# Performance work log

Measured on AMD Instinct MI355X. Metric: run time of the kernel, lower is better.

## Reference

```python
import jax, jax.numpy as jnp
import numpy as np

H = 256        # h_dim
ATTN = 3       # attn_len (structurally fixed: 3 modality pairs / 3 unimodal streams)


def lstm_scan(x, Wih, Whh, b, h0, c0):
    """Standard LSTM (PyTorch gate order i,f,g,o) over time. x: (B,T,D) -> (B,T,H)."""
    def step(carry, xt):
        h, c = carry
        g = xt @ Wih + h @ Whh + b
        i, f, gg, o = jnp.split(g, 4, axis=-1)
        c = jax.nn.sigmoid(f) * c + jax.nn.sigmoid(i) * jnp.tanh(gg)
        h = jax.nn.sigmoid(o) * jnp.tanh(c)
        return (h, c), h
    _, hs = jax.lax.scan(step, (h0, c0), jnp.swapaxes(x, 0, 1))
    return jnp.swapaxes(hs, 0, 1)


def pad_shift(x, shift, padv=0.0):
    """Shift 3D tensor (B,T,D) forward in time by `shift` with constant padding."""
    pad = jnp.full((x.shape[0], shift, x.shape[2]), padv, x.dtype)
    return jnp.concatenate([pad, x[:, :-shift, :]], axis=1)


def setup_inputs() -> dict:
    key = jax.random.key(0)
    ks = jax.random.split(key, 24)
    B, T = 16, 1024
    F, A, Tx = 512, 256, 768
    s = jnp.float32(0.05)
    f32 = jnp.float32
    inp = {
        "x": jax.random.normal(ks[0], (B, T, 1), f32),
        "face_features": jax.random.normal(ks[1], (B, T, F), f32),
        "audio_features": jax.random.normal(ks[2], (B, T, A), f32),
        "text_features": jax.random.normal(ks[3], (B, T, Tx), f32),
        "target": jax.random.normal(ks[4], (B, T, 1), f32),
        "text_W": jax.random.normal(ks[5], (Tx, H), f32) * s,
        "text_b": jnp.zeros((H,), f32),
        "face_W": jax.random.normal(ks[6], (F, H), f32) * s,
        "face_b": jnp.zeros((H,), f32),
        "audio_W": jax.random.normal(ks[7], (A, H), f32) * s,
        "audio_b": jnp.zeros((H,), f32),
        "att_W": jax.random.normal(ks[8], (2 * H,), f32) * s,
        "att_b": jnp.zeros((), f32),
        "ut_W": jax.random.normal(ks[9], (H,), f32) * s,
        "ut_b": jnp.zeros((), f32),
        "uf_W": jax.random.normal(ks[10], (H,), f32) * s,
        "uf_b": jnp.zeros((), f32),
        "ua_W": jax.random.normal(ks[11], (H,), f32) * s,
        "ua_b": jnp.zeros((), f32),
        "enc_Wih": jax.random.normal(ks[12], (ATTN, ATTN, 4 * H), f32) * s,
        "enc_Whh": jax.random.normal(ks[13], (ATTN, H, 4 * H), f32) * s,
        "enc_b": jnp.zeros((ATTN, 4 * H), f32),
        "enc_outW": jax.random.normal(ks[14], (ATTN, H), f32) * s,
        "enc_outb": jnp.zeros((ATTN,), f32),
        "dec_Wih": jax.random.normal(ks[15], (1 + ATTN, 4 * H), f32) * s,
        "dec_Whh": jax.random.normal(ks[16], (H, 4 * H), f32) * s,
        "dec_b": jnp.zeros((4 * H,), f32),
        "dec_h0": jnp.zeros((H,), f32),
        "dec_c0": jnp.zeros((H,), f32),
        "out1_W": jax.random.normal(ks[17], (H, 4), f32) * s,
        "out1_b": jnp.zeros((4,), f32),
        "out2_W": jax.random.normal(ks[18], (4, 1), f32) * s,
        "out2_b": jnp.zeros((1,), f32),
    }
    return inp


def reference(x, face_features, audio_features, text_features, target,
              text_W, text_b, face_W, face_b, audio_W, audio_b,
              att_W, att_b, ut_W, ut_b, uf_W, uf_b, ua_W, ua_b,
              enc_Wih, enc_Whh, enc_b, enc_outW, enc_outb,
              dec_Wih, dec_Whh, dec_b, dec_h0, dec_c0,
              out1_W, out1_b, out2_W, out2_b):
    B, T = x.shape[0], x.shape[1]
    tr = text_features @ text_W + text_b    # (B,T,H)
    fr = face_features @ face_W + face_b
    ar = audio_features @ audio_W + audio_b

    def pair_att(a, b2):  # Linear(2H->1) on tanh(cat), softmax over TIME
        s = jnp.tanh(jnp.concatenate([a, b2], axis=-1)) @ att_W + att_b  # (B,T)
        return jax.nn.softmax(s, axis=-1)

    def uni(rep, W, bb):  # Linear(H->1) on tanh(rep), softmax over TIME
        return jax.nn.softmax(jnp.tanh(rep) @ W + bb, axis=-1)  # (B,T)

    att1 = pair_att(tr, fr); att2 = pair_att(fr, ar); att3 = pair_att(tr, ar)
    enc_input = jnp.concatenate([uni(tr, ut_W, ut_b), uni(fr, uf_W, uf_b),
                                 uni(ar, ua_W, ua_b)], axis=-1).reshape(B, T, ATTN)
    attn = jnp.concatenate([att1, att2, att3], axis=-1).reshape(B, T, ATTN)

    # cLSTM shared encoder: ATTN independent LSTMs over the full 3-dim input,
    # each followed by Linear(H->1); outputs concatenated -> (B,T,ATTN).
    z0 = jnp.zeros((B, H), enc_input.dtype)
    hs = jax.vmap(lambda Wih, Whh, bb: lstm_scan(enc_input, Wih, Whh, bb, z0, z0))(
        enc_Wih, enc_Whh, enc_b)                      # (ATTN,B,T,H)
    enc_out = jnp.einsum('kbth,kh->btk', hs, enc_outW) + enc_outb  # (B,T,ATTN)

    # convolve: local causal weighted sum over ATTN shifted copies
    shifted = jnp.stack([enc_out if i == 0 else pad_shift(enc_out, i)
                         for i in range(ATTN)], axis=-1)           # (B,T,ATTN,ATTN)
    context = jnp.sum(attn[:, :, None, :] * shifted, axis=-1)      # (B,T,ATTN)

    # decoder (teacher forcing path)
    dec_in = jnp.concatenate([pad_shift(target, 1, 0.0), context], axis=2)  # (B,T,1+ATTN)
    dh0 = jnp.tile(dec_h0[None], (B, 1))
    dc0 = jnp.tile(dec_c0[None], (B, 1))
    dec_out = lstm_scan(dec_in, dec_Wih, dec_Whh, dec_b, dh0, dc0)  # (B,T,H)
    predicted = jax.nn.relu(dec_out @ out1_W + out1_b) @ out2_W + out2_b  # (B,T,1)
    return predicted
```

## Files before the change

kernel.cpp:

```cpp
#include <hip/hip_runtime.h>
#include <hip/hip_bf16.h>

typedef float f32x4 __attribute__((ext_vector_type(4)));
typedef __bf16 bf16x8 __attribute__((ext_vector_type(8)));
typedef unsigned long long ull;

#define DEVI static __device__ __forceinline__

DEVI unsigned f2bfu(float f){
  unsigned u = __builtin_bit_cast(unsigned, f);
  return (u + 0x7fffu + ((u >> 16) & 1u)) >> 16;
}
DEVI float bf2f(unsigned s){
  return __builtin_bit_cast(float, s << 16);
}
DEVI float sigf(float x){ return 1.f/(1.f + __expf(-x)); }
DEVI float thf(float x){ return 2.f*sigf(2.f*x) - 1.f; }

DEVI ull allc(const ull* p){
  return __hip_atomic_load(p, __ATOMIC_RELAXED, __HIP_MEMORY_SCOPE_AGENT);
}
DEVI void alst(ull* p, ull v){
  __hip_atomic_store(p, v, __ATOMIC_RELAXED, __HIP_MEMORY_SCOPE_AGENT);
}

__global__ __launch_bounds__(256) void k_pack_lstm(
    const float* __restrict__ encWhh, const float* __restrict__ encWih,
    const float* __restrict__ decWhh, const float* __restrict__ decWih,
    const float* __restrict__ encB,   const float* __restrict__ decB,
    unsigned short* __restrict__ outp)
{
  const int total = 4*16*9*4*64*8;
  for (int e = blockIdx.x*blockDim.x + threadIdx.x; e < total; e += gridDim.x*blockDim.x){
    int j  = e & 7;
    int l  = (e >> 3) & 63;
    int g  = (e >> 9) & 3;
    int r  = e >> 11;
    int kt = r % 9;  r /= 9;
    int w  = r & 15;
    int lstm = r >> 4;
    int k = 32*kt + 8*(l >> 4) + j;
    int n = 256*g + 16*w + (l & 15);
    float v = 0.f;
    if (lstm < 3){
      if (k < 256)       v = encWhh[(lstm*256 + k)*1024 + n];
      else if (k < 259)  v = encWih[(lstm*3 + (k-256))*1024 + n];
      else if (k == 260) v = encB[lstm*1024 + n];
    } else {
      if (k < 256)       v = decWhh[k*1024 + n];
      else if (k < 260)  v = decWih[(k-256)*1024 + n];
      else if (k == 260) v = decB[n];
    }
    outp[e] = (unsigned short)f2bfu(v);
  }
}

__global__ __launch_bounds__(256) void k_pack_B(
    const float* __restrict__ W, int KT, unsigned short* __restrict__ outp)
{
  const int total = 2*KT*8*64*8;
  for (int e = blockIdx.x*blockDim.x + threadIdx.x; e < total; e += gridDim.x*blockDim.x){
    int j  = e & 7;
    int l  = (e >> 3) & 63;
    int nt = (e >> 9) & 7;
    int r  = e >> 12;
    int kt = r % KT;
    int tn = r / KT;
    int k = 32*kt + 8*(l >> 4) + j;
    int n = 128*tn + 16*nt + (l & 15);
    outp[e] = (unsigned short)f2bfu(W[k*256 + n]);
  }
}

__global__ __launch_bounds__(256) void k_proj(
    const float* __restrict__ A, const unsigned short* __restrict__ Bp,
    const float* __restrict__ bias, unsigned short* __restrict__ outT, int K)
{
  __shared__ unsigned char sA[8192];
  __shared__ unsigned char sB[8192];
  const int tid = threadIdx.x;
  const int l = tid & 63;
  const int wv = tid >> 6;
  const int wm = wv >> 1, wn = wv & 1;
  const int tm = blockIdx.x, tn = blockIdx.y;
  const int KT = K >> 5;

  f32x4 acc[4][4];
  #pragma unroll
  for (int a = 0; a < 4; ++a)
    #pragma unroll
    for (int cc = 0; cc < 4; ++cc)
      acc[a][cc] = f32x4{0.f,0.f,0.f,0.f};

  const int arow = tid >> 1;
  const float* Ap = A + (size_t)(tm*128 + arow)*K + (tid & 1)*16;
  const uint4* Bsrc = (const uint4*)Bp + (size_t)tn*KT*512 + tid*2;

  for (int kt = 0; kt < KT; ++kt){
    float4 f0 = *(const float4*)(Ap + kt*32);
    float4 f1 = *(const float4*)(Ap + kt*32 + 4);
    float4 f2 = *(const float4*)(Ap + kt*32 + 8);
    float4 f3 = *(const float4*)(Ap + kt*32 + 12);
    uint4 p0, p1;
    p0.x = f2bfu(f0.x) | (f2bfu(f0.y) << 16);
    p0.y = f2bfu(f0.z) | (f2bfu(f0.w) << 16);
    p0.z = f2bfu(f1.x) | (f2bfu(f1.y) << 16);
    p0.w = f2bfu(f1.z) | (f2bfu(f1.w) << 16);
    p1.x = f2bfu(f2.x) | (f2bfu(f2.y) << 16);
    p1.y = f2bfu(f2.z) | (f2bfu(f2.w) << 16);
    p1.z = f2bfu(f3.x) | (f2bfu(f3.y) << 16);
    p1.w = f2bfu(f3.z) | (f2bfu(f3.w) << 16);
    unsigned base = arow*64 + (tid & 1)*32;
    unsigned sw = (arow & 3) << 4;
    *(uint4*)(sA + ((base)      ^ sw)) = p0;
    *(uint4*)(sA + ((base + 16) ^ sw)) = p1;
    *((uint4*)sB + tid*2)     = Bsrc[kt*512];
    *((uint4*)sB + tid*2 + 1) = Bsrc[kt*512 + 1];
    __syncthreads();

    bf16x8 af[4], bf[4];
    #pragma unroll
    for (int a = 0; a < 4; ++a){
      unsigned row = 64*wm + 16*a + (l & 15);
      unsigned off = (row*64 + 16*(l >> 4)) ^ ((row & 3) << 4);
      af[a] = __builtin_bit_cast(bf16x8, *(const uint4*)(sA + off));
    }
    #pragma unroll
    for (int cc = 0; cc < 4; ++cc){
      unsigned off = ((4*wn + cc)*64 + l)*16;
      bf[cc] = __builtin_bit_cast(bf16x8, *(const uint4*)(sB + off));
    }
    #pragma unroll
    for (int a = 0; a < 4; ++a)
      #pragma unroll
      for (int cc = 0; cc < 4; ++cc)
        acc[a][cc] = __builtin_amdgcn_mfma_f32_16x16x32_bf16(af[a], bf[cc], acc[a][cc], 0, 0, 0);
    __syncthreads();
  }
  #pragma unroll
  for (int cc = 0; cc < 4; ++cc){
    int colg = tn*128 + 64*wn + 16*cc + (l & 15);
    float bs = bias[colg];
    #pragma unroll
    for (int a = 0; a < 4; ++a){
      int rowg = tm*128 + 64*wm + 16*a + 4*(l >> 4);
      #pragma unroll
      for (int r = 0; r < 4; ++r){
        outT[(size_t)(rowg + r)*256 + colg] = (unsigned short)f2bfu(thf(acc[a][cc][r] + bs));
      }
    }
  }
}

__global__ __launch_bounds__(256) void k_attdot(
    const unsigned short* __restrict__ tT, const unsigned short* __restrict__ tF,
    const unsigned short* __restrict__ tA,
    const float* __restrict__ attW, const float* __restrict__ utW,
    const float* __restrict__ ufW, const float* __restrict__ uaW,
    float* __restrict__ s6)
{
  const int l = threadIdx.x & 63;
  const int wid = (blockIdx.x*blockDim.x + threadIdx.x) >> 6;
  const int nw = (gridDim.x*blockDim.x) >> 6;
  float alo[4], ahi[4], wt[4], wf[4], wa[4];
  #pragma unroll
  for (int q = 0; q < 4; ++q){
    alo[q] = attW[4*l + q];
    ahi[q] = attW[256 + 4*l + q];
    wt[q]  = utW[4*l + q];
    wf[q]  = ufW[4*l + q];
    wa[q]  = uaW[4*l + q];
  }
  for (int r = wid; r < 16384; r += nw){
    uint2 vT = *(const uint2*)(tT + (size_t)r*256 + 4*l);
    uint2 vF = *(const uint2*)(tF + (size_t)r*256 + 4*l);
    uint2 vA = *(const uint2*)(tA + (size_t)r*256 + 4*l);
    float xt[4] = { bf2f(vT.x & 0xffff), bf2f(vT.x >> 16), bf2f(vT.y & 0xffff), bf2f(vT.y >> 16) };
    float xf[4] = { bf2f(vF.x & 0xffff), bf2f(vF.x >> 16), bf2f(vF.y & 0xffff), bf2f(vF.y >> 16) };
    float xa[4] = { bf2f(vA.x & 0xffff), bf2f(vA.x >> 16), bf2f(vA.y & 0xffff), bf2f(vA.y >> 16) };
    float ptlo = 0.f, ptu = 0.f, pflo = 0.f, pfhi = 0.f, pfu = 0.f, pahi = 0.f, pau = 0.f;
    #pragma unroll
    for (int q = 0; q < 4; ++q){
      ptlo += xt[q]*alo[q]; ptu += xt[q]*wt[q];
      pflo += xf[q]*alo[q]; pfhi += xf[q]*ahi[q]; pfu += xf[q]*wf[q];
      pahi += xa[q]*ahi[q]; pau += xa[q]*wa[q];
    }
    #pragma unroll
    for (int s = 1; s < 64; s <<= 1){
      ptlo += __shfl_xor(ptlo, s); ptu  += __shfl_xor(ptu, s);
      pflo += __shfl_xor(pflo, s); pfhi += __shfl_xor(pfhi, s);
      pfu  += __shfl_xor(pfu, s);  pahi += __shfl_xor(pahi, s);
      pau  += __shfl_xor(pau, s);
    }
    if (l == 0){
      int o = r;
      s6[o]             = ptlo + pfhi;
      s6[16384 + o]     = pflo + pahi;
      s6[2*16384 + o]   = ptlo + pahi;
      s6[3*16384 + o]   = ptu;
      s6[4*16384 + o]   = pfu;
      s6[5*16384 + o]   = pau;
    }
  }
}

__global__ __launch_bounds__(256) void k_zerofeed(unsigned short* __restrict__ encfeed)
{
  int i = blockIdx.x*blockDim.x + threadIdx.x;
  if (i < 16384) encfeed[i*4 + 3] = 0;
}

__global__ __launch_bounds__(256) void k_zerows(uint4* __restrict__ p, int n)
{
  for (int i = blockIdx.x*blockDim.x + threadIdx.x; i < n; i += gridDim.x*blockDim.x)
    p[i] = uint4{0u,0u,0u,0u};
}

__global__ __launch_bounds__(256) void k_smax(
    const float* __restrict__ s6, float* __restrict__ attn_tb,
    unsigned short* __restrict__ encfeed)
{
  __shared__ float red[4];
  const int f = blockIdx.x >> 4;
  const int b = blockIdx.x & 15;
  const int tid = threadIdx.x;
  const float* row = s6 + f*16384 + b*1024;
  float4 v = *(const float4*)(row + 4*tid);
  float mx = fmaxf(fmaxf(v.x, v.y), fmaxf(v.z, v.w));
  #pragma unroll
  for (int s = 1; s < 64; s <<= 1) mx = fmaxf(mx, __shfl_xor(mx, s));
  if ((tid & 63) == 0) red[tid >> 6] = mx;
  __syncthreads();
  mx = fmaxf(fmaxf(red[0], red[1]), fmaxf(red[2], red[3]));
  float e0 = __expf(v.x - mx), e1 = __expf(v.y - mx), e2 = __expf(v.z - mx), e3 = __expf(v.w - mx);
  float sm = e0 + e1 + e2 + e3;
  __syncthreads();
  #pragma unroll
  for (int s = 1; s < 64; s <<= 1) sm += __shfl_xor(sm, s);
  if ((tid & 63) == 0) red[tid >> 6] = sm;
  __syncthreads();
  sm = red[0] + red[1] + red[2] + red[3];
  float inv = 1.f/sm;
  float e[4] = {e0, e1, e2, e3};
  int ff = (f < 3) ? f : f - 3;
  #pragma unroll
  for (int q = 0; q < 4; ++q){
    int idx = ff*1024 + 4*tid + q;
    int tt = idx/3, kk = idx - 3*tt;
    if (f < 3) attn_tb[(tt*16 + b)*3 + kk] = e[q]*inv;
    else       encfeed[(tt*16 + b)*4 + kk] = (unsigned short)f2bfu(e[q]*inv);
  }
}

__global__ __launch_bounds__(512, 2) void k_lstm(
    const unsigned short* __restrict__ packW,
    const unsigned short* __restrict__ encfeed,
    const float* __restrict__ target,
    const float* __restrict__ attn_tb,
    const float* __restrict__ encOutW,
    const float* __restrict__ encOutB,
    const float* __restrict__ dec_h0,
    const float* __restrict__ dec_c0,
    unsigned short* __restrict__ dec_h,
    ull* __restrict__ exch,
    ull* __restrict__ partials)
{
  __shared__ unsigned char hl[2][16*768];
  __shared__ float ring[3][16][3];
  __shared__ float eo_part[2][48];
  const int tid = threadIdx.x;
  const int l = tid & 63;
  const int w = tid >> 6;
  const int pair = blockIdx.x >> 1;
  const int half = blockIdx.x & 1;
  const int wglob = half*8 + w;
  const bool isdec = (pair == 3);

  const int b = l & 15;
  const int j0 = 16*wglob + 4*(l >> 4);
  const unsigned swb = (unsigned)(b & 7) << 4;

  float c[4];
  #pragma unroll
  for (int r = 0; r < 4; ++r) c[r] = isdec ? dec_c0[j0 + r] : 0.f;

  float wow[4] = {0.f, 0.f, 0.f, 0.f};
  if (!isdec){
    #pragma unroll
    for (int r = 0; r < 4; ++r) wow[r] = encOutW[pair*256 + j0 + r];
  }
  float eb[3] = {0.f, 0.f, 0.f};
  if (isdec && tid < 16){
    #pragma unroll
    for (int k = 0; k < 3; ++k) eb[k] = encOutB[k];
  }

  {
    int ib = tid >> 5;
    int ic = (tid & 31) * 8;
    #pragma unroll
    for (int q = 0; q < 2; ++q){
      int c0 = ic + 4*q;
      uint2 hz;
      if (isdec){
        hz.x = f2bfu(dec_h0[c0])   | (f2bfu(dec_h0[c0+1]) << 16);
        hz.y = f2bfu(dec_h0[c0+2]) | (f2bfu(dec_h0[c0+3]) << 16);
      } else { hz.x = 0u; hz.y = 0u; }
      *(uint2*)(hl[0] + ((ib*768 + 2*c0) ^ ((unsigned)(ib & 7) << 4))) = hz;
    }
  }
  if (tid < 224){
    int bufi = tid / 112;
    int r = tid % 112;
    int bb = r / 7, q = r % 7;
    uint2 z;
    z.x = (q == 0) ? 0x00003f80u : 0u;
    z.y = 0u;
    *(uint2*)(hl[bufi] + ((bb*768 + 520 + 8*q) ^ ((unsigned)(bb & 7) << 4))) = z;
  }
  if (!isdec && tid < 16){
    uint2 gx0 = *(const uint2*)(encfeed + tid*4);
    *(uint2*)(hl[0] + ((tid*768 + 512) ^ ((unsigned)(tid & 7) << 4))) = gx0;
  }

  const uint4* wb = (const uint4*)packW + ((size_t)(pair*16 + wglob)*36)*64 + l;
  uint4 wreg[36];
  #pragma unroll
  for (int i = 0; i < 36; ++i) wreg[i] = wb[i*64];
  #pragma unroll
  for (int i = 0; i < 36; ++i){
    unsigned t0 = wreg[i].x, t1 = wreg[i].y, t2 = wreg[i].z, t3 = wreg[i].w;
    asm volatile("" : "+a"(t0), "+a"(t1), "+a"(t2), "+a"(t3));
    wreg[i].x = t0; wreg[i].y = t1; wreg[i].z = t2; wreg[i].w = t3;
  }

  if (isdec){
    if (tid < 96){
      int bb = tid & 15, kk = (tid >> 4) % 3, h2 = tid / 48;
      const ull* p8 = partials + (((size_t)0*3 + kk)*2 + h2)*128 + bb;
      ull v[8];
      #pragma unroll
      for (int wv = 0; wv < 8; ++wv) v[wv] = allc(p8 + wv*16);
      bool ok = false;
      while (!ok){
        ok = true;
        #pragma unroll
        for (int wv = 0; wv < 8; ++wv)
          if ((unsigned)(v[wv] >> 32) != 1u){ v[wv] = allc(p8 + wv*16); ok = false; }
      }
      float s = 0.f;
      #pragma unroll
      for (int wv = 0; wv < 8; ++wv) s += __builtin_bit_cast(float, (unsigned)v[wv]);
      eo_part[h2][kk*16 + bb] = s;
    }
    __syncthreads();
    if (tid < 16){
      int bb = tid;
      float a0 = attn_tb[bb*3 + 0];
      unsigned ok3[3];
      #pragma unroll
      for (int k = 0; k < 3; ++k){
        float eo = eb[k] + eo_part[0][k*16 + bb] + eo_part[1][k*16 + bb];
        ring[0][bb][k] = eo; ring[1][bb][k] = 0.f; ring[2][bb][k] = 0.f;
        ok3[k] = f2bfu(a0*eo);
      }
      uint2 pk; pk.x = (ok3[0] << 16); pk.y = ok3[1] | (ok3[2] << 16);
      *(uint2*)(hl[0] + ((bb*768 + 512) ^ ((unsigned)(bb & 7) << 4))) = pk;
    }
  }
  __syncthreads();

  for (int t = 0; t < 1024; ++t){
    const int p = t + 1;
    const unsigned char* cur = hl[t & 1];
    unsigned char* nxt = (unsigned char*)hl[p & 1];

    bf16x8 af[9];
    #pragma unroll
    for (int kt = 0; kt < 9; ++kt){
      unsigned off = (unsigned)(b*768 + kt*64 + 16*(l >> 4)) ^ swb;
      af[kt] = __builtin_bit_cast(bf16x8, *(const uint4*)(cur + off));
    }

    uint2 gx;
    const bool ldx = (!isdec) && (t < 1023) && (tid < 16);
    if (ldx) gx = *(const uint2*)(encfeed + (size_t)p*64 + tid*4);
    float at0 = 0.f, at1 = 0.f, at2 = 0.f, tg = 0.f;
    const bool bld = isdec && (t < 1023) && (tid < 16);
    if (bld){
      at0 = attn_tb[((size_t)p*16 + tid)*3 + 0];
      at1 = attn_tb[((size_t)p*16 + tid)*3 + 1];
      at2 = attn_tb[((size_t)p*16 + tid)*3 + 2];
      tg  = target[tid*1024 + t];
    }

    f32x4 acc[4];
    #pragma unroll
    for (int g = 0; g < 4; ++g) acc[g] = f32x4{0.f,0.f,0.f,0.f};
    #pragma unroll
    for (int kt = 0; kt < 9; ++kt){
      #pragma unroll
      for (int g = 0; g < 4; ++g)
        acc[g] = __builtin_amdgcn_mfma_f32_16x16x32_bf16(
            __builtin_bit_cast(bf16x8, wreg[kt*4 + g]), af[kt], acc[g], 0, 0, 0);
    }

    unsigned hp[4];
    #pragma unroll
    for (int r = 0; r < 4; ++r){
      float vi = sigf(acc[0][r]);
      float vf = sigf(acc[1][r]);
      float vg = thf (acc[2][r]);
      float vo = sigf(acc[3][r]);
      float cc = vf*c[r] + vi*vg;
      c[r] = cc;
      hp[r] = f2bfu(vo * thf(cc));
    }
    uint2 hpk; hpk.x = hp[0] | (hp[1] << 16); hpk.y = hp[2] | (hp[3] << 16);
    *(uint2*)(nxt + ((b*768 + 2*j0) ^ swb)) = hpk;

    if (isdec){
      *(uint2*)(dec_h + (size_t)(t*16 + b)*256 + j0) = hpk;
    } else {
      float s = bf2f(hp[0])*wow[0] + bf2f(hp[1])*wow[1]
              + bf2f(hp[2])*wow[2] + bf2f(hp[3])*wow[3];
      s += __shfl_xor(s, 16);
      s += __shfl_xor(s, 32);
      if (l < 16)
        alst(partials + (((size_t)t*3 + pair)*2 + half)*128 + w*16 + l,
             ((ull)(unsigned)p << 32) | (ull)__builtin_bit_cast(unsigned, s));
    }

    if (t < 1023){
      {
        size_t xs = ((((size_t)pair*2 + (p & 1))*2 + half)*16 + b)*64
                  + ((unsigned)(j0 & 127) >> 1);
        alst(exch + xs,     ((ull)(unsigned)p << 32) | (ull)hpk.x);
        alst(exch + xs + 1, ((ull)(unsigned)p << 32) | (ull)hpk.y);
      }
      const int pb2 = tid >> 5, pj = tid & 31;
      const ull* rb = exch + ((((size_t)pair*2 + (p & 1))*2 + (half^1))*16 + pb2)*64 + pj*2;
      ull v0 = allc(rb), v1 = allc(rb + 1);
      const bool pol = isdec && (tid < 96);
      const int kk = (tid >> 4) % 3, h2 = tid / 48, bb = tid & 15;
      const ull* p8 = partials + (((size_t)p*3 + kk)*2 + h2)*128 + bb;
      ull pv[8];
      if (pol){
        #pragma unroll
        for (int wv = 0; wv < 8; ++wv) pv[wv] = allc(p8 + wv*16);
      }
      while (((unsigned)(v0 >> 32) != (unsigned)p) || ((unsigned)(v1 >> 32) != (unsigned)p)){
        if ((unsigned)(v0 >> 32) != (unsigned)p) v0 = allc(rb);
        if ((unsigned)(v1 >> 32) != (unsigned)p) v1 = allc(rb + 1);
      }
      uint2 pk2; pk2.x = (unsigned)v0; pk2.y = (unsigned)v1;
      *(uint2*)(nxt + ((pb2*768 + 256*(half^1) + 8*pj) ^ ((unsigned)(pb2 & 7) << 4))) = pk2;
      if (pol){
        const unsigned want = (unsigned)(p + 1);
        bool ok = false;
        while (!ok){
          ok = true;
          #pragma unroll
          for (int wv = 0; wv < 8; ++wv)
            if ((unsigned)(pv[wv] >> 32) != want){ pv[wv] = allc(p8 + wv*16); ok = false; }
        }
        float s2 = 0.f;
        #pragma unroll
        for (int wv = 0; wv < 8; ++wv) s2 += __builtin_bit_cast(float, (unsigned)pv[wv]);
        eo_part[h2][kk*16 + bb] = s2;
      }
      if (ldx) *(uint2*)(nxt + ((tid*768 + 512) ^ ((unsigned)(tid & 7) << 4))) = gx;
      __syncthreads();
      if (isdec){
        if (tid < 16){
          int s0 = p % 3, s1 = (p + 2) % 3, s2i = (p + 1) % 3;
          unsigned ok3[3];
          #pragma unroll
          for (int k = 0; k < 3; ++k){
            float eo = eb[k] + eo_part[0][k*16 + tid] + eo_part[1][k*16 + tid];
            ring[s0][tid][k] = eo;
            ok3[k] = f2bfu(at0*eo + at1*ring[s1][tid][k] + at2*ring[s2i][tid][k]);
          }
          uint2 pk3; pk3.x = f2bfu(tg) | (ok3[0] << 16); pk3.y = ok3[1] | (ok3[2] << 16);
          *(uint2*)(nxt + ((tid*768 + 512) ^ ((unsigned)(tid & 7) << 4))) = pk3;
        }
        __syncthreads();
      }
    }
  }
}

__global__ __launch_bounds__(256) void k_decout(
    const unsigned short* __restrict__ dec_h, const float* __restrict__ W1,
    const float* __restrict__ b1, const float* __restrict__ W2,
    const float* __restrict__ b2, float* __restrict__ out)
{
  const int l = threadIdx.x & 63;
  const int wid = (blockIdx.x*blockDim.x + threadIdx.x) >> 6;
  const int nw = (gridDim.x*blockDim.x) >> 6;
  const int o = l >> 4, jc = l & 15;
  for (int e = wid; e < 16384; e += nw){
    int t = e >> 4, b = e & 15;
    const unsigned short* hr = dec_h + (size_t)(t*16 + b)*256 + jc*16;
    uint4 v0 = *(const uint4*)hr;
    uint4 v1 = *(const uint4*)(hr + 8);
    unsigned vv[8] = {v0.x, v0.y, v0.z, v0.w, v1.x, v1.y, v1.z, v1.w};
    float p = 0.f;
    #pragma unroll
    for (int q = 0; q < 8; ++q){
      int j = jc*16 + 2*q;
      p += bf2f(vv[q] & 0xffff) * W1[j*4 + o];
      p += bf2f(vv[q] >> 16)    * W1[(j + 1)*4 + o];
    }
    p += __shfl_xor(p, 1); p += __shfl_xor(p, 2);
    p += __shfl_xor(p, 4); p += __shfl_xor(p, 8);
    float v = 0.f;
    if (jc == 0) v = fmaxf(p + b1[o], 0.f) * W2[o];
    v += __shfl_xor(v, 16);
    v += __shfl_xor(v, 32);
    if (l == 0) out[b*1024 + t] = v + b2[0];
  }
}

extern "C" void kernel_launch(void* const* d_in, const int* in_sizes, int n_in,
                              void* d_out, int out_size, void* d_ws, size_t ws_size,
                              hipStream_t stream)
{
  const float* faceF   = (const float*)d_in[1];
  const float* audioF  = (const float*)d_in[2];
  const float* textF   = (const float*)d_in[3];
  const float* target  = (const float*)d_in[4];
  const float* textW   = (const float*)d_in[5];
  const float* textB   = (const float*)d_in[6];
  const float* faceW   = (const float*)d_in[7];
  const float* faceB   = (const float*)d_in[8];
  const float* audioW  = (const float*)d_in[9];
  const float* audioB  = (const float*)d_in[10];
  const float* attW    = (const float*)d_in[11];
  const float* utW     = (const float*)d_in[13];
  const float* ufW     = (const float*)d_in[15];
  const float* uaW     = (const float*)d_in[17];
  const float* encWih  = (const float*)d_in[19];
  const float* encWhh  = (const float*)d_in[20];
  const float* encB    = (const float*)d_in[21];
  const float* encOutW = (const float*)d_in[22];
  const float* encOutB = (const float*)d_in[23];
  const float* decWih  = (const float*)d_in[24];
  const float* decWhh  = (const float*)d_in[25];
  const float* decB    = (const float*)d_in[26];
  const float* decH0   = (const float*)d_in[27];
  const float* decC0   = (const float*)d_in[28];
  const float* out1W   = (const float*)d_in[29];
  const float* out1B   = (const float*)d_in[30];
  const float* out2W   = (const float*)d_in[31];
  const float* out2B   = (const float*)d_in[32];
  float* out = (float*)d_out;

  char* ws = (char*)d_ws;
  size_t off = 0;
  auto alloc = [&](size_t bytes) -> void* {
    void* p = ws + off;
    off += (bytes + 255) & ~(size_t)255;
    return p;
  };
  unsigned short* packL   = (unsigned short*)alloc(1179648ull*2);
  unsigned short* packT   = (unsigned short*)alloc(196608ull*2);
  unsigned short* packF   = (unsigned short*)alloc(131072ull*2);
  unsigned short* packA   = (unsigned short*)alloc(65536ull*2);
  unsigned short* tanhT   = (unsigned short*)alloc(16384ull*256*2);
  unsigned short* tanhF   = (unsigned short*)alloc(16384ull*256*2);
  unsigned short* tanhA   = (unsigned short*)alloc(16384ull*256*2);
  float*          s6      = (float*)alloc(6ull*16384*4);
  float*          attn_tb = (float*)alloc(49152ull*4);
  unsigned short* encfeed = (unsigned short*)alloc(65536ull*2);
  unsigned short* dec_h   = (unsigned short*)alloc(1024ull*16*256*2);
  ull*            exch    = (ull*)alloc(16384ull*8);
  ull*            partials= (ull*)alloc(786432ull*8);
  if (off > ws_size) return;

  hipLaunchKernelGGL(k_pack_lstm, dim3(512), dim3(256), 0, stream,
                     encWhh, encWih, decWhh, decWih, encB, decB, packL);
  hipLaunchKernelGGL(k_pack_B, dim3(256), dim3(256), 0, stream, textW, 24, packT);
  hipLaunchKernelGGL(k_pack_B, dim3(256), dim3(256), 0, stream, faceW, 16, packF);
  hipLaunchKernelGGL(k_pack_B, dim3(128), dim3(256), 0, stream, audioW, 8, packA);
  hipLaunchKernelGGL(k_zerows, dim3(1024), dim3(256), 0, stream,
                     (uint4*)exch, (int)((16384ull*8 + 786432ull*8) / 16));

  hipLaunchKernelGGL(k_proj, dim3(128, 2), dim3(256), 0, stream, textF,  packT, textB,  tanhT, 768);
  hipLaunchKernelGGL(k_proj, dim3(128, 2), dim3(256), 0, stream, faceF,  packF, faceB,  tanhF, 512);
  hipLaunchKernelGGL(k_proj, dim3(128, 2), dim3(256), 0, stream, audioF, packA, audioB, tanhA, 256);

  hipLaunchKernelGGL(k_attdot, dim3(256), dim3(256), 0, stream,
                     tanhT, tanhF, tanhA, attW, utW, ufW, uaW, s6);
  hipLaunchKernelGGL(k_zerofeed, dim3(64), dim3(256), 0, stream, encfeed);
  hipLaunchKernelGGL(k_smax, dim3(96), dim3(256), 0, stream, s6, attn_tb, encfeed);

  hipLaunchKernelGGL(k_lstm, dim3(8), dim3(512), 0, stream,
                     packL, encfeed, target, attn_tb, encOutW, encOutB,
                     decH0, decC0, dec_h, exch, partials);
  hipLaunchKernelGGL(k_decout, dim3(256), dim3(256), 0, stream,
                     dec_h, out1W, out1B, out2W, out2B, out);
}
```

Measured before the change: 4.852 ms.

## Overlap partner-half hidden-state exchange with own-half MFMA work

Each block now starts the recurrent matmul on the K tiles it produced itself, plus the input tile, before waiting for the partner block's half of the hidden state. Only then does it spin on the exchange buffer, write the partner data into the current LDS buffer, sync, and finish the remaining K tiles. The aim is to hide the cross-block handoff latency behind local MFMA work. It adds an extra __syncthreads per step and moves the exchange polling to the next iteration, which could add overhead if the handoff is already fast.

```diff
diff --git a/kernel.cpp b/kernel.cpp
--- a/kernel.cpp
+++ b/kernel.cpp
@@ -273,11 +273,10 @@
   const int w = tid >> 6;
   const int pair = blockIdx.x >> 1;
   const int half = blockIdx.x & 1;
-  const int wglob = half*8 + w;
   const bool isdec = (pair == 3);
 
   const int b = l & 15;
-  const int j0 = 16*wglob + 4*(l >> 4);
+  const int j0 = 16*(half*8 + w) + 4*(l >> 4);
   const unsigned swb = (unsigned)(b & 7) << 4;
 
   float c[4];
@@ -323,7 +322,7 @@
     *(uint2*)(hl[0] + ((tid*768 + 512) ^ ((unsigned)(tid & 7) << 4))) = gx0;
   }
 
-  const uint4* wb = (const uint4*)packW + ((size_t)(pair*16 + wglob)*36)*64 + l;
+  const uint4* wb = (const uint4*)packW + ((size_t)(pair*16 + half*8 + w)*36)*64 + l;
   uint4 wreg[36];
   #pragma unroll
   for (int i = 0; i < 36; ++i) wreg[i] = wb[i*64];
@@ -370,16 +369,30 @@
   }
   __syncthreads();
 
+  const int ktOwn = half*4;
+  const int ktPar = (half^1)*4;
+
   for (int t = 0; t < 1024; ++t){
     const int p = t + 1;
-    const unsigned char* cur = hl[t & 1];
+    unsigned char* cur = (unsigned char*)hl[t & 1];
     unsigned char* nxt = (unsigned char*)hl[p & 1];
 
-    bf16x8 af[9];
-    #pragma unroll
-    for (int kt = 0; kt < 9; ++kt){
-      unsigned off = (unsigned)(b*768 + kt*64 + 16*(l >> 4)) ^ swb;
-      af[kt] = __builtin_bit_cast(bf16x8, *(const uint4*)(cur + off));
+    const int pb2 = tid >> 5, pj = tid & 31;
+    const ull* rb = exch + ((((size_t)pair*2 + (t & 1))*2 + (half^1))*16 + pb2)*64 + pj*2;
+    ull v0 = 0, v1 = 0;
+    if (t > 0){ v0 = allc(rb); v1 = allc(rb + 1); }
+
+    ull ev0, ev1, ev2;
+    const ull* pe = partials;
+    const bool pol = isdec && (t < 1023) && (tid < 96);
+    const int kk = (tid >> 4) % 3, h2 = tid / 48, bb96 = tid & 15;
+    if (pol){
+      pe = partials + (((size_t)p*3 + kk)*2 + h2)*128 + bb96;
+    }
+    ull pv[8];
+    if (pol){
+      #pragma unroll
+      for (int wv = 0; wv < 8; ++wv) pv[wv] = allc(pe + wv*16);
     }
 
     uint2 gx;
@@ -398,11 +411,42 @@
     #pragma unroll
     for (int g = 0; g < 4; ++g) acc[g] = f32x4{0.f,0.f,0.f,0.f};
     #pragma unroll
-    for (int kt = 0; kt < 9; ++kt){
+    for (int i = 0; i < 4; ++i){
+      unsigned off = (unsigned)(b*768 + (ktOwn + i)*64 + 16*(l >> 4)) ^ swb;
+      bf16x8 a = __builtin_bit_cast(bf16x8, *(const uint4*)(cur + off));
       #pragma unroll
       for (int g = 0; g < 4; ++g)
         acc[g] = __builtin_amdgcn_mfma_f32_16x16x32_bf16(
-            __builtin_bit_cast(bf16x8, wreg[kt*4 + g]), af[kt], acc[g], 0, 0, 0);
+            __builtin_bit_cast(bf16x8, wreg[(ktOwn + i)*4 + g]), a, acc[g], 0, 0, 0);
+    }
+    {
+      unsigned off = (unsigned)(b*768 + 8*64 + 16*(l >> 4)) ^ swb;
+      bf16x8 a = __builtin_bit_cast(bf16x8, *(const uint4*)(cur + off));
+      #pragma unroll
+      for (int g = 0; g < 4; ++g)
+        acc[g] = __builtin_amdgcn_mfma_f32_16x16x32_bf16(
+            __builtin_bit_cast(bf16x8, wreg[8*4 + g]), a, acc[g], 0, 0, 0);
+    }
+
+    if (t > 0){
+      const unsigned want = (unsigned)t;
+      while (((unsigned)(v0 >> 32) != want) || ((unsigned)(v1 >> 32) != want)){
+        if ((unsigned)(v0 >> 32) != want) v0 = allc(rb);
+        if ((unsigned)(v1 >> 32) != want) v1 = allc(rb + 1);
+      }
+      uint2 pk2; pk2.x = (unsigned)v0; pk2.y = (unsigned)v1;
+      *(uint2*)(cur + ((pb2*768 + 256*(half^1) + 8*pj) ^ ((unsigned)(pb2 & 7) << 4))) = pk2;
+    }
+    __syncthreads();
+
+    #pragma unroll
+    for (int i = 0; i < 4; ++i){
+      unsigned off = (unsigned)(b*768 + (ktPar + i)*64 + 16*(l >> 4)) ^ swb;
+      bf16x8 a = __builtin_bit_cast(bf16x8, *(const uint4*)(cur + off));
+      #pragma unroll
+      for (int g = 0; g < 4; ++g)
+        acc[g] = __builtin_amdgcn_mfma_f32_16x16x32_bf16(
+            __builtin_bit_cast(bf16x8, wreg[(ktPar + i)*4 + g]), a, acc[g], 0, 0, 0);
     }
 
     unsigned hp[4];
@@ -432,29 +476,11 @@
     }
 
     if (t < 1023){
-      {
-        size_t xs = ((((size_t)pair*2 + (p & 1))*2 + half)*16 + b)*64
-                  + ((unsigned)(j0 & 127) >> 1);
-        alst(exch + xs,     ((ull)(unsigned)p << 32) | (ull)hpk.x);
-        alst(exch + xs + 1, ((ull)(unsigned)p << 32) | (ull)hpk.y);
-      }
-      const int pb2 = tid >> 5, pj = tid & 31;
-      const ull* rb = exch + ((((size_t)pair*2 + (p & 1))*2 + (half^1))*16 + pb2)*64 + pj*2;
-      ull v0 = allc(rb), v1 = allc(rb + 1);
-      const bool pol = isdec && (tid < 96);
-      const int kk = (tid >> 4) % 3, h2 = tid / 48, bb = tid & 15;
-      const ull* p8 = partials + (((size_t)p*3 + kk)*2 + h2)*128 + bb;
-      ull pv[8];
-      if (pol){
-        #pragma unroll
-        for (int wv = 0; wv < 8; ++wv) pv[wv] = allc(p8 + wv*16);
-      }
-      while (((unsigned)(v0 >> 32) != (unsigned)p) || ((unsigned)(v1 >> 32) != (unsigned)p)){
-        if ((unsigned)(v0 >> 32) != (unsigned)p) v0 = allc(rb);
-        if ((unsigned)(v1 >> 32) != (unsigned)p) v1 = allc(rb + 1);
-      }
-      uint2 pk2; pk2.x = (unsigned)v0; pk2.y = (unsigned)v1;
-      *(uint2*)(nxt + ((pb2*768 + 256*(half^1) + 8*pj) ^ ((unsigned)(pb2 & 7) << 4))) = pk2;
+      size_t xs = ((((size_t)pair*2 + (p & 1))*2 + half)*16 + b)*64
+                + ((unsigned)(j0 & 127) >> 1);
+      alst(exch + xs,     ((ull)(unsigned)p << 32) | (ull)hpk.x);
+      alst(exch + xs + 1, ((ull)(unsigned)p << 32) | (ull)hpk.y);
+
       if (pol){
         const unsigned want = (unsigned)(p + 1);
         bool ok = false;
@@ -462,12 +488,12 @@
           ok = true;
           #pragma unroll
           for (int wv = 0; wv < 8; ++wv)
-            if ((unsigned)(pv[wv] >> 32) != want){ pv[wv] = allc(p8 + wv*16); ok = false; }
+            if ((unsigned)(pv[wv] >> 32) != want){ pv[wv] = allc(pe + wv*16); ok = false; }
         }
         float s2 = 0.f;
         #pragma unroll
         for (int wv = 0; wv < 8; ++wv) s2 += __builtin_bit_cast(float, (unsigned)pv[wv]);
-        eo_part[h2][kk*16 + bb] = s2;
+        eo_part[h2][kk*16 + bb96] = s2;
       }
       if (ldx) *(uint2*)(nxt + ((tid*768 + 512) ^ ((unsigned)(tid & 7) << 4))) = gx;
       __syncthreads();
```

Result: slower. 10.22 ms (+110.7%).
